# Performance work log

Hardware: AMD Instinct MI355X
Metric: run time of the kernel (lower is better)

Reference implementation:

```python
import jax, jax.numpy as jnp
import numpy as np

N_USER, N_MOVIE, E, H, L = 100000, 20000, 1000000, 64, 2
NEG_SLOPE = 0.2  # PyG GATv2Conv default negative_slope


def _rand_edges(k, n_src, n_dst, e):
    k1, k2 = jax.random.split(k)
    src = jax.random.randint(k1, (e,), 0, n_src, dtype=jnp.int32)
    dst = jax.random.randint(k2, (e,), 0, n_dst, dtype=jnp.int32)
    # ensure no src==dst index collisions so PyG's remove_self_loops is a no-op
    dst = jnp.where(dst == src, (dst + 1) % n_dst, dst)
    return jnp.stack([src, dst])


def setup_inputs() -> dict:
    key = jax.random.key(0)
    ks = jax.random.split(key, 8)
    return {
        "x_user": jax.random.normal(ks[0], (N_USER, H), jnp.float32),
        "x_movie": jax.random.normal(ks[1], (N_MOVIE, H), jnp.float32),
        "edge_u2m": _rand_edges(ks[2], N_USER, N_MOVIE, E),
        "edge_m2u": _rand_edges(ks[3], N_MOVIE, N_USER, E),
        # params stacked as [layer, edge_type, ...]; edge_type 0 = user->movie, 1 = movie->user
        "Wl": jax.random.normal(ks[4], (L, 2, H, H), jnp.float32) / np.sqrt(H).astype(np.float32),
        "bl": jnp.zeros((L, 2, H), jnp.float32),
        "Wr": jax.random.normal(ks[5], (L, 2, H, H), jnp.float32) / np.sqrt(H).astype(np.float32),
        "br": jnp.zeros((L, 2, H), jnp.float32),
        "att": jax.random.normal(ks[6], (L, 2, H), jnp.float32) / np.sqrt(H).astype(np.float32),
        "bias": jnp.zeros((L, 2, H), jnp.float32),
    }


def _segment_softmax(scores, seg, n):
    # numerically-stable softmax over variable-degree dst neighborhoods (PyG softmax)
    m = jax.ops.segment_max(scores, seg, num_segments=n)
    ex = jnp.exp(scores - m[seg])
    s = jax.ops.segment_sum(ex, seg, num_segments=n)
    return ex / (s[seg] + 1e-16)


def _gatv2(x_src, x_dst, edge, Wl, bl, Wr, br, att, bias):
    n_src, n_dst = x_src.shape[0], x_dst.shape[0]
    xl = x_src @ Wl + bl  # [N_src, H]
    xr = x_dst @ Wr + br  # [N_dst, H]
    n_loop = min(n_src, n_dst)  # PyG adds self loops with num_nodes = min(N_src, N_dst)
    loop = jnp.arange(n_loop, dtype=edge.dtype)
    src = jnp.concatenate([edge[0], loop])
    dst = jnp.concatenate([edge[1], loop])
    e = jax.nn.leaky_relu(xl[src] + xr[dst], NEG_SLOPE)  # [E', H] gathered per edge
    score = e @ att  # [E']
    alpha = _segment_softmax(score, dst, n_dst)
    out = jax.ops.segment_sum(xl[src] * alpha[:, None], dst, num_segments=n_dst)
    return out + bias


def reference(x_user, x_movie, edge_u2m, edge_m2u, Wl, bl, Wr, br, att, bias):
    for l in range(L):
        new_movie = _gatv2(x_user, x_movie, edge_u2m,
                           Wl[l, 0], bl[l, 0], Wr[l, 0], br[l, 0], att[l, 0], bias[l, 0])
        new_user = _gatv2(x_movie, x_user, edge_m2u,
                          Wl[l, 1], bl[l, 1], Wr[l, 1], br[l, 1], att[l, 1], bias[l, 1])
        x_movie = jax.nn.selu(new_movie)
        x_user = jax.nn.selu(new_user)
    return x_user, x_movie
```

## Files before the change

kernel.cpp:

```cpp
#include <hip/hip_runtime.h>
#include <hip/hip_fp16.h>
#include <cstdint>

#define H 64
#define EPR 16
#define NB 120

__device__ __forceinline__ float selu_f(float x) {
  const float sc = 1.0507009873554805f;
  const float al = 1.6732632423543772f;
  return x > 0.f ? sc * x : sc * al * (expf(x) - 1.f);
}

__global__ __launch_bounds__(256) void gemm64_dual(
    const float* __restrict__ A,
    const float* __restrict__ W0, const float* __restrict__ b0,
    const float* __restrict__ W1, const float* __restrict__ b1,
    __half* __restrict__ C0, float* __restrict__ C1, int N) {
  __shared__ float Ws0[64 * 64];
  __shared__ float Ws1[64 * 64];
  __shared__ float As[64][65];
  __shared__ float bs0[64], bs1[64];

  const int tid = threadIdx.x;
  for (int i = tid; i < 1024; i += 256) {
    ((float4*)Ws0)[i] = ((const float4*)W0)[i];
    ((float4*)Ws1)[i] = ((const float4*)W1)[i];
  }
  if (tid < 64) { bs0[tid] = b0[tid]; bs1[tid] = b1[tid]; }

  const int row0 = blockIdx.x * 64;
  for (int i = tid; i < 1024; i += 256) {
    int r = i >> 4, c4 = i & 15;
    int row = row0 + r;
    float4 v = make_float4(0.f, 0.f, 0.f, 0.f);
    if (row < N) v = ((const float4*)(A + (size_t)row * H))[c4];
    As[r][c4 * 4 + 0] = v.x;
    As[r][c4 * 4 + 1] = v.y;
    As[r][c4 * 4 + 2] = v.z;
    As[r][c4 * 4 + 3] = v.w;
  }
  __syncthreads();

  const int g = tid & 3;
  const int r = tid >> 2;
  float a0[16], a1[16];
#pragma unroll
  for (int j = 0; j < 16; ++j) { a0[j] = bs0[g * 16 + j]; a1[j] = bs1[g * 16 + j]; }

  for (int k = 0; k < 64; ++k) {
    float ak = As[r][k];
    const float4* w0r = (const float4*)&Ws0[k * 64 + g * 16];
    const float4* w1r = (const float4*)&Ws1[k * 64 + g * 16];
#pragma unroll
    for (int j4 = 0; j4 < 4; ++j4) {
      float4 w0 = w0r[j4], w1 = w1r[j4];
      a0[j4 * 4 + 0] += ak * w0.x; a0[j4 * 4 + 1] += ak * w0.y;
      a0[j4 * 4 + 2] += ak * w0.z; a0[j4 * 4 + 3] += ak * w0.w;
      a1[j4 * 4 + 0] += ak * w1.x; a1[j4 * 4 + 1] += ak * w1.y;
      a1[j4 * 4 + 2] += ak * w1.z; a1[j4 * 4 + 3] += ak * w1.w;
    }
  }

  const int row = row0 + r;
  if (row < N) {
    unsigned pu[8];
#pragma unroll
    for (int j2 = 0; j2 < 8; ++j2) {
      __half2 t = __floats2half2_rn(a0[2 * j2], a0[2 * j2 + 1]);
      pu[j2] = *(unsigned*)&t;
    }
    uint4* c0 = (uint4*)(C0 + (size_t)row * H + g * 16);
    c0[0] = make_uint4(pu[0], pu[1], pu[2], pu[3]);
    c0[1] = make_uint4(pu[4], pu[5], pu[6], pu[7]);

    float4* c1 = (float4*)(C1 + (size_t)row * H + g * 16);
#pragma unroll
    for (int j4 = 0; j4 < 4; ++j4) {
      c1[j4] = make_float4(a1[j4 * 4 + 0], a1[j4 * 4 + 1], a1[j4 * 4 + 2], a1[j4 * 4 + 3]);
    }
  }
}

__global__ __launch_bounds__(256) void bucket_hist(
    const int* __restrict__ ed1, int E1r, int n1e, int sh1, int B1, int* __restrict__ mat1,
    const int* __restrict__ ed2, int E2r, int n2e, int sh2, int B2, int* __restrict__ mat2) {
  __shared__ int hist[256];
  int b = blockIdx.x;
  const int* ed; int Er, ne, sh, Bn, blk; int* mat;
  if (b < NB) { ed = ed1; Er = E1r; ne = n1e; sh = sh1; Bn = B1; mat = mat1; blk = b; }
  else { ed = ed2; Er = E2r; ne = n2e; sh = sh2; Bn = B2; mat = mat2; blk = b - NB; }
  for (int i = threadIdx.x; i < Bn; i += 256) hist[i] = 0;
  __syncthreads();
  int chunk = (ne + NB - 1) / NB;
  int lo = blk * chunk, hi = lo + chunk;
  if (hi > ne) hi = ne;
  for (int e = lo + threadIdx.x; e < hi; e += 256) {
    int d = (e < Er) ? ed[e] : (e - Er);
    atomicAdd(&hist[d >> sh], 1);
  }
  __syncthreads();
  for (int i = threadIdx.x; i < Bn; i += 256) mat[(size_t)i * NB + blk] = hist[i];
}

__global__ __launch_bounds__(256) void scan_partial2(
    const int* __restrict__ cnt1, int n1, int* __restrict__ psum1, int* __restrict__ bsum1,
    const int* __restrict__ cnt2, int n2, int* __restrict__ psum2, int* __restrict__ bsum2,
    int split) {
  __shared__ int sh[256];
  int b = blockIdx.x;
  const int* cnt; int n; int* psum; int* bsum; int lb;
  if (b < split) { cnt = cnt1; n = n1; psum = psum1; bsum = bsum1; lb = b; }
  else { cnt = cnt2; n = n2; psum = psum2; bsum = bsum2; lb = b - split; }
  int i = lb * 256 + threadIdx.x;
  int tid = threadIdx.x;
  sh[tid] = (i < n) ? cnt[i] : 0;
  __syncthreads();
  for (int off = 1; off < 256; off <<= 1) {
    int t = (tid >= off) ? sh[tid - off] : 0;
    __syncthreads();
    if (tid >= off) sh[tid] += t;
    __syncthreads();
  }
  if (i < n) psum[i] = sh[tid];
  if (tid == 255) bsum[lb] = sh[255];
}

__global__ __launch_bounds__(256) void scan_bsums2(
    int* __restrict__ bsum1, int nb1, int* __restrict__ bsum2, int nb2) {
  __shared__ int sh[256];
  const int tid = threadIdx.x;
  for (int which = 0; which < 2; ++which) {
    int* bsum = which ? bsum2 : bsum1;
    int nb = which ? nb2 : nb1;
    int run = 0;
    for (int start = 0; start < nb; start += 256) {
      int i = start + tid;
      int v = (i < nb) ? bsum[i] : 0;
      __syncthreads();
      sh[tid] = v;
      __syncthreads();
      for (int off = 1; off < 256; off <<= 1) {
        int t = (tid >= off) ? sh[tid - off] : 0;
        __syncthreads();
        if (tid >= off) sh[tid] += t;
        __syncthreads();
      }
      if (i < nb) bsum[i] = run + sh[tid] - v;
      run += sh[255];
      __syncthreads();
    }
  }
}

__global__ __launch_bounds__(256) void finalize_excl2(
    const int* __restrict__ cnt1, const int* __restrict__ psum1,
    const int* __restrict__ bsum1, int n1, int* __restrict__ excl1,
    const int* __restrict__ cnt2, const int* __restrict__ psum2,
    const int* __restrict__ bsum2, int n2, int* __restrict__ excl2, int split) {
  int b = blockIdx.x;
  const int *cnt, *psum, *bsum; int n; int* excl; int lb;
  if (b < split) { cnt = cnt1; psum = psum1; bsum = bsum1; n = n1; excl = excl1; lb = b; }
  else { cnt = cnt2; psum = psum2; bsum = bsum2; n = n2; excl = excl2; lb = b - split; }
  int i = lb * 256 + threadIdx.x;
  if (i >= n) return;
  excl[i] = psum[i] + bsum[lb] - cnt[i];
}

__global__ __launch_bounds__(256) void bucket_part(
    const int* __restrict__ es1, const int* __restrict__ ed1, int E1r, int n1e,
    int sh1, int B1, const int* __restrict__ excl1, unsigned* __restrict__ part1,
    const int* __restrict__ es2, const int* __restrict__ ed2, int E2r, int n2e,
    int sh2, int B2, const int* __restrict__ excl2, unsigned* __restrict__ part2) {
  __shared__ int cur[256];
  int b = blockIdx.x;
  const int *es, *ed, *excl; int Er, ne, sh, Bn, blk; unsigned* part;
  if (b < NB) { es = es1; ed = ed1; Er = E1r; ne = n1e; sh = sh1; Bn = B1; excl = excl1; part = part1; blk = b; }
  else { es = es2; ed = ed2; Er = E2r; ne = n2e; sh = sh2; Bn = B2; excl = excl2; part = part2; blk = b - NB; }
  for (int i = threadIdx.x; i < Bn; i += 256) cur[i] = excl[(size_t)i * NB + blk];
  __syncthreads();
  int chunk = (ne + NB - 1) / NB;
  int lo = blk * chunk, hi = lo + chunk;
  if (hi > ne) hi = ne;
  const unsigned lmask = (1u << sh) - 1u;
  for (int e = lo + threadIdx.x; e < hi; e += 256) {
    int s, d;
    if (e < Er) { s = es[e]; d = ed[e]; } else { s = e - Er; d = s; }
    int bkt = d >> sh;
    int pos = atomicAdd(&cur[bkt], 1);
    part[pos] = (((unsigned)d & lmask) << 18) | (unsigned)s;
  }
}

__global__ __launch_bounds__(256) void bucket_sort(
    const unsigned* __restrict__ part1, const int* __restrict__ excl1,
    int n1e, int sh1, int B1, int nd1, int* __restrict__ rp1, int* __restrict__ csr1,
    const unsigned* __restrict__ part2, const int* __restrict__ excl2,
    int n2e, int sh2, int B2, int nd2, int* __restrict__ rp2, int* __restrict__ csr2) {
  __shared__ int cnt_s[512];
  __shared__ int scan_s[512];
  int b = blockIdx.x;
  const unsigned* part; const int* excl; int ne, sh, Bn, nd, bkt; int *rp, *csr;
  if (b < B1) { part = part1; excl = excl1; ne = n1e; sh = sh1; Bn = B1; nd = nd1; rp = rp1; csr = csr1; bkt = b; }
  else { part = part2; excl = excl2; ne = n2e; sh = sh2; Bn = B2; nd = nd2; rp = rp2; csr = csr2; bkt = b - B1; }
  const int tid = threadIdx.x;
  const int dbase = bkt << sh;
  const int R = 1 << sh;
  int rcap = nd - dbase;
  if (rcap > R) rcap = R;
  const int base = excl[(size_t)bkt * NB];
  const int endv = (bkt == Bn - 1) ? ne : excl[(size_t)(bkt + 1) * NB];

  cnt_s[tid] = 0; cnt_s[256 + tid] = 0;
  __syncthreads();
  for (int i = base + tid; i < endv; i += 256)
    atomicAdd(&cnt_s[part[i] >> 18], 1);
  __syncthreads();
  scan_s[tid] = cnt_s[tid];
  scan_s[256 + tid] = cnt_s[256 + tid];
  __syncthreads();
  for (int off = 1; off < 256; off <<= 1) {
    int t = (tid >= off) ? scan_s[tid - off] : 0;
    __syncthreads();
    if (tid >= off) scan_s[tid] += t;
    __syncthreads();
  }
  for (int off = 1; off < 256; off <<= 1) {
    int t = (tid >= off) ? scan_s[256 + tid - off] : 0;
    __syncthreads();
    if (tid >= off) scan_s[256 + tid] += t;
    __syncthreads();
  }
  int lowtot = scan_s[255];
  scan_s[256 + tid] += lowtot;
  __syncthreads();
  if (tid < rcap) rp[dbase + tid + 1] = base + scan_s[tid];
  if (256 + tid < rcap) rp[dbase + 256 + tid + 1] = base + scan_s[256 + tid];
  cnt_s[tid] = base + scan_s[tid] - cnt_s[tid];
  cnt_s[256 + tid] = base + scan_s[256 + tid] - cnt_s[256 + tid];
  if (tid == 0 && bkt == 0) rp[0] = 0;
  __syncthreads();
  for (int i = base + tid; i < endv; i += 256) {
    unsigned p = part[i];
    int dl = p >> 18;
    int pos = atomicAdd(&cnt_s[dl], 1);
    csr[pos] = (int)(p & 0x3FFFFu);
  }
}

__global__ __launch_bounds__(256) void gat_dst(
    const int* __restrict__ row_ptr, const int* __restrict__ csr_src,
    const __half* __restrict__ xl, const float* __restrict__ xr,
    const float* __restrict__ att, const float* __restrict__ bias,
    float* __restrict__ out, int n_dst) {
  __shared__ __align__(16) float tile[4][EPR * 64];

  const int w = threadIdx.x >> 6;
  const int d = blockIdx.x * 4 + w;
  if (d >= n_dst) return;
  const int h = threadIdx.x & 63;
  float* tl = tile[w];

  const float xr_h = xr[(size_t)d * H + h];
  const float att_h = att[h];
  const int beg = row_ptr[d];
  const int end = row_ptr[d + 1];

  const int r = h & 15;
  const int q = h >> 4;

  float m = -3.0e38f, s = 0.f, acc = 0.f;

  for (int base = beg; base < end; base += EPR) {
    int cnt = end - base;
    if (cnt > EPR) cnt = EPR;
    float v[EPR];

#pragma unroll
    for (int qq = 0; qq < EPR / 4; ++qq) {
      if (qq * 4 < cnt) {
#pragma unroll
        for (int i = 0; i < 4; ++i) {
          const int k = qq * 4 + i;
          int j = k < cnt ? k : cnt - 1;
          int src = csr_src[base + j];
          float vv = __half2float(xl[(size_t)src * H + h]);
          v[k] = vv;
          float p = vv + xr_h;
          p = fmaxf(p, 0.f) + 0.2f * fminf(p, 0.f);
          tl[(k << 6) + ((((h >> 2) ^ k) << 2) | (h & 3))] = p * att_h;
        }
      }
    }

    const float4* t4 = (const float4*)tl;
    float t0 = 0.f, t1 = 0.f, t2 = 0.f, t3 = 0.f;
#pragma unroll
    for (int c = 0; c < 4; ++c) {
      float4 q4 = t4[(r << 4) + (((q << 2) + c) ^ r)];
      t0 += q4.x; t1 += q4.y; t2 += q4.z; t3 += q4.w;
    }
    float t = (t0 + t1) + (t2 + t3);
    t += __shfl_xor(t, 16, 64);
    t += __shfl_xor(t, 32, 64);
    t = (r < cnt) ? t : -3.0e38f;

    float M = t;
#pragma unroll
    for (int mk = 1; mk <= 8; mk <<= 1) M = fmaxf(M, __shfl_xor(M, mk, 64));
    float e = __expf(t - M);
    float S = e;
#pragma unroll
    for (int mk = 1; mk <= 8; mk <<= 1) S += __shfl_xor(S, mk, 64);
    if (h < 16) tl[h] = e;

    float nm = fmaxf(m, M);
    float a_old = __expf(m - nm);
    float a_new = __expf(M - nm);
    float P = 0.f;
#pragma unroll
    for (int qq = 0; qq < EPR / 4; ++qq) {
      if (qq * 4 < cnt) {
        float4 w4 = ((const float4*)tl)[qq];
        P += w4.x * v[qq * 4 + 0];
        P += w4.y * v[qq * 4 + 1];
        P += w4.z * v[qq * 4 + 2];
        P += w4.w * v[qq * 4 + 3];
      }
    }
    s = s * a_old + S * a_new;
    acc = acc * a_old + P * a_new;
    m = nm;
  }

  float o = acc / (s + 1e-16f) + bias[h];
  out[(size_t)d * H + h] = selu_f(o);
}

extern "C" void kernel_launch(void* const* d_in, const int* in_sizes, int n_in,
                              void* d_out, int out_size, void* d_ws, size_t ws_size,
                              hipStream_t stream) {
  const float* x_user = (const float*)d_in[0];
  const float* x_movie = (const float*)d_in[1];
  const int* e_u2m = (const int*)d_in[2];
  const int* e_m2u = (const int*)d_in[3];
  const float* Wl = (const float*)d_in[4];
  const float* bl = (const float*)d_in[5];
  const float* Wr = (const float*)d_in[6];
  const float* br = (const float*)d_in[7];
  const float* att = (const float*)d_in[8];
  const float* bias = (const float*)d_in[9];

  const int n_user = in_sizes[0] / H;
  const int n_movie = in_sizes[1] / H;
  const int E1 = in_sizes[2] / 2;
  const int E2 = in_sizes[3] / 2;
  const int n_loop = n_user < n_movie ? n_user : n_movie;
  const int nE1 = E1 + n_loop;
  const int nE2 = E2 + n_loop;

  const int SHM = 7, SHU = 9;
  const int Bm = (n_movie + (1 << SHM) - 1) >> SHM;
  const int Bu = (n_user + (1 << SHU) - 1) >> SHU;
  const int nmatM = Bm * NB, nmatU = Bu * NB;
  const int nbm = (nmatM + 255) / 256, nbu = (nmatU + 255) / 256;

  float* ws = (float*)d_ws;
  size_t o = 0;
  __half* xl_u2m = (__half*)(ws + o); o += (size_t)n_user * H / 2;
  __half* xl_m2u = (__half*)(ws + o); o += (size_t)n_movie * H / 2;
  float* xr_u2m = ws + o; o += (size_t)n_movie * H;
  float* xr_m2u = ws + o; o += (size_t)n_user * H;

  int* matM  = (int*)(ws + o); o += nmatM;
  int* psumM = (int*)(ws + o); o += nmatM;
  int* exclM = (int*)(ws + o); o += nmatM;
  int* matU  = (int*)(ws + o); o += nmatU;
  int* psumU = (int*)(ws + o); o += nmatU;
  int* exclU = (int*)(ws + o); o += nmatU;
  int* bsumM = (int*)(ws + o); o += 1024;
  int* bsumU = (int*)(ws + o); o += 1024;
  unsigned* partM = (unsigned*)(ws + o); o += nE1;
  unsigned* partU = (unsigned*)(ws + o); o += nE2;
  int* csr1 = (int*)(ws + o); o += nE1;
  int* csr2 = (int*)(ws + o); o += nE2;
  int* rp1  = (int*)(ws + o); o += n_movie + 1;
  int* rp2  = (int*)(ws + o); o += n_user + 1;

  float* out_u = (float*)d_out;
  float* out_m = out_u + (size_t)n_user * H;

  const int gu = (n_user + 63) / 64;
  const int gm = (n_movie + 63) / 64;

  bucket_hist<<<2 * NB, 256, 0, stream>>>(
      e_u2m + E1, E1, nE1, SHM, Bm, matM,
      e_m2u + E2, E2, nE2, SHU, Bu, matU);
  scan_partial2<<<nbm + nbu, 256, 0, stream>>>(
      matM, nmatM, psumM, bsumM, matU, nmatU, psumU, bsumU, nbm);
  scan_bsums2<<<1, 256, 0, stream>>>(bsumM, nbm, bsumU, nbu);
  finalize_excl2<<<nbm + nbu, 256, 0, stream>>>(
      matM, psumM, bsumM, nmatM, exclM,
      matU, psumU, bsumU, nmatU, exclU, nbm);
  bucket_part<<<2 * NB, 256, 0, stream>>>(
      e_u2m, e_u2m + E1, E1, nE1, SHM, Bm, exclM, partM,
      e_m2u, e_m2u + E2, E2, nE2, SHU, Bu, exclU, partU);
  bucket_sort<<<Bm + Bu, 256, 0, stream>>>(
      partM, exclM, nE1, SHM, Bm, n_movie, rp1, csr1,
      partU, exclU, nE2, SHU, Bu, n_user, rp2, csr2);

  for (int l = 0; l < 2; ++l) {
    const float* cu = (l == 0) ? x_user : out_u;
    const float* cm = (l == 0) ? x_movie : out_m;
    const int p0 = l * 2 + 0;
    const int p1 = l * 2 + 1;

    gemm64_dual<<<gu, 256, 0, stream>>>(
        cu, Wl + (size_t)p0 * H * H, bl + (size_t)p0 * H,
        Wr + (size_t)p1 * H * H, br + (size_t)p1 * H, xl_u2m, xr_m2u, n_user);
    gemm64_dual<<<gm, 256, 0, stream>>>(
        cm, Wl + (size_t)p1 * H * H, bl + (size_t)p1 * H,
        Wr + (size_t)p0 * H * H, br + (size_t)p0 * H, xl_m2u, xr_u2m, n_movie);

    gat_dst<<<(n_movie + 3) / 4, 256, 0, stream>>>(
        rp1, csr1, xl_u2m, xr_u2m, att + (size_t)p0 * H, bias + (size_t)p0 * H, out_m, n_movie);
    gat_dst<<<(n_user + 3) / 4, 256, 0, stream>>>(
        rp2, csr2, xl_m2u, xr_m2u, att + (size_t)p1 * H, bias + (size_t)p1 * H, out_u, n_user);
  }
}
```

Baseline: 531.5 us.

## Merge per-direction GEMM and GAT launches into single kernels, simplify leaky-relu

Both gemm64_dual calls are fused into one launch and both gat_dst calls into one launch, with each block choosing its edge direction by block index. This cuts launch count and lets the smaller movie-side work fill the GPU alongside the user side, removing tail idle time between launches. Inside the GAT kernel the leaky-relu-times-att is rewritten as a single fma with an abs term, the source index is made wave-uniform via readfirstlane, and the swizzle index math is simplified. The cost is extra pointer selection per block and some divergence in register pressure between the two branches.

```diff
diff --git a/kernel.cpp b/kernel.cpp
--- a/kernel.cpp
+++ b/kernel.cpp
@@ -12,16 +12,30 @@
   return x > 0.f ? sc * x : sc * al * (expf(x) - 1.f);
 }
 
-__global__ __launch_bounds__(256) void gemm64_dual(
-    const float* __restrict__ A,
-    const float* __restrict__ W0, const float* __restrict__ b0,
-    const float* __restrict__ W1, const float* __restrict__ b1,
-    __half* __restrict__ C0, float* __restrict__ C1, int N) {
+__global__ __launch_bounds__(256) void gemm64_dual2(
+    const float* __restrict__ Au, const float* __restrict__ Am,
+    const float* __restrict__ W0u, const float* __restrict__ b0u,
+    const float* __restrict__ W1u, const float* __restrict__ b1u,
+    const float* __restrict__ W0m, const float* __restrict__ b0m,
+    const float* __restrict__ W1m, const float* __restrict__ b1m,
+    __half* __restrict__ C0u, float* __restrict__ C1u,
+    __half* __restrict__ C0m, float* __restrict__ C1m,
+    int Nu, int Nm, int split) {
   __shared__ float Ws0[64 * 64];
   __shared__ float Ws1[64 * 64];
   __shared__ float As[64][65];
   __shared__ float bs0[64], bs1[64];
 
+  const float *A, *W0, *b0, *W1, *b1;
+  __half* C0; float* C1; int N, blk;
+  if (blockIdx.x < split) {
+    A = Au; W0 = W0u; b0 = b0u; W1 = W1u; b1 = b1u;
+    C0 = C0u; C1 = C1u; N = Nu; blk = blockIdx.x;
+  } else {
+    A = Am; W0 = W0m; b0 = b0m; W1 = W1m; b1 = b1m;
+    C0 = C0m; C1 = C1m; N = Nm; blk = blockIdx.x - split;
+  }
+
   const int tid = threadIdx.x;
   for (int i = tid; i < 1024; i += 256) {
     ((float4*)Ws0)[i] = ((const float4*)W0)[i];
@@ -29,7 +43,7 @@
   }
   if (tid < 64) { bs0[tid] = b0[tid]; bs1[tid] = b1[tid]; }
 
-  const int row0 = blockIdx.x * 64;
+  const int row0 = blk * 64;
   for (int i = tid; i < 1024; i += 256) {
     int r = i >> 4, c4 = i & 15;
     int row = row0 + r;
@@ -248,26 +262,43 @@
   }
 }
 
-__global__ __launch_bounds__(256) void gat_dst(
-    const int* __restrict__ row_ptr, const int* __restrict__ csr_src,
-    const __half* __restrict__ xl, const float* __restrict__ xr,
-    const float* __restrict__ att, const float* __restrict__ bias,
-    float* __restrict__ out, int n_dst) {
+__global__ __launch_bounds__(256) void gat_dst2(
+    const int* __restrict__ rp1, const int* __restrict__ csr1,
+    const __half* __restrict__ xl1, const float* __restrict__ xr1,
+    const float* __restrict__ att1, const float* __restrict__ bias1,
+    float* __restrict__ out1, int nd1,
+    const int* __restrict__ rp2, const int* __restrict__ csr2,
+    const __half* __restrict__ xl2, const float* __restrict__ xr2,
+    const float* __restrict__ att2, const float* __restrict__ bias2,
+    float* __restrict__ out2, int nd2, int split) {
   __shared__ __align__(16) float tile[4][EPR * 64];
 
+  const int b = blockIdx.x;
+  const int* rp; const int* csr; const __half* xl; const float *xr, *att, *bias;
+  float* out; int nd, d0;
+  if (b < split) {
+    rp = rp1; csr = csr1; xl = xl1; xr = xr1; att = att1; bias = bias1;
+    out = out1; nd = nd1; d0 = b * 4;
+  } else {
+    rp = rp2; csr = csr2; xl = xl2; xr = xr2; att = att2; bias = bias2;
+    out = out2; nd = nd2; d0 = (b - split) * 4;
+  }
   const int w = threadIdx.x >> 6;
-  const int d = blockIdx.x * 4 + w;
-  if (d >= n_dst) return;
+  const int d = d0 + w;
+  if (d >= nd) return;
   const int h = threadIdx.x & 63;
   float* tl = tile[w];
 
   const float xr_h = xr[(size_t)d * H + h];
-  const float att_h = att[h];
-  const int beg = row_ptr[d];
-  const int end = row_ptr[d + 1];
+  const float a = att[h];
+  const float a06 = 0.6f * a, a04 = 0.4f * a;
+  const float bias_h = bias[h];
+  const int beg = rp[d];
+  const int end = rp[d + 1];
 
   const int r = h & 15;
   const int q = h >> 4;
+  const int pr = (q << 2) ^ r;
 
   float m = -3.0e38f, s = 0.f, acc = 0.f;
 
@@ -283,12 +314,13 @@
         for (int i = 0; i < 4; ++i) {
           const int k = qq * 4 + i;
           int j = k < cnt ? k : cnt - 1;
-          int src = csr_src[base + j];
-          float vv = __half2float(xl[(size_t)src * H + h]);
+          int src = __builtin_amdgcn_readfirstlane(csr[base + j]);
+          const __half* row = xl + ((size_t)src << 6);
+          float vv = __half2float(row[h]);
           v[k] = vv;
           float p = vv + xr_h;
-          p = fmaxf(p, 0.f) + 0.2f * fminf(p, 0.f);
-          tl[(k << 6) + ((((h >> 2) ^ k) << 2) | (h & 3))] = p * att_h;
+          float c = fmaf(p, a06, fabsf(p) * a04);
+          tl[(k << 6) | (h ^ (k << 2))] = c;
         }
       }
     }
@@ -297,7 +329,7 @@
     float t0 = 0.f, t1 = 0.f, t2 = 0.f, t3 = 0.f;
 #pragma unroll
     for (int c = 0; c < 4; ++c) {
-      float4 q4 = t4[(r << 4) + (((q << 2) + c) ^ r)];
+      float4 q4 = t4[(r << 4) | (pr ^ c)];
       t0 += q4.x; t1 += q4.y; t2 += q4.z; t3 += q4.w;
     }
     float t = (t0 + t1) + (t2 + t3);
@@ -333,7 +365,7 @@
     m = nm;
   }
 
-  float o = acc / (s + 1e-16f) + bias[h];
+  float o = acc / (s + 1e-16f) + bias_h;
   out[(size_t)d * H + h] = selu_f(o);
 }
 
@@ -392,6 +424,8 @@
 
   const int gu = (n_user + 63) / 64;
   const int gm = (n_movie + 63) / 64;
+  const int split1 = (n_movie + 3) / 4;
+  const int split2 = (n_user + 3) / 4;
 
   bucket_hist<<<2 * NB, 256, 0, stream>>>(
       e_u2m + E1, E1, nE1, SHM, Bm, matM,
@@ -415,16 +449,19 @@
     const int p0 = l * 2 + 0;
     const int p1 = l * 2 + 1;
 
-    gemm64_dual<<<gu, 256, 0, stream>>>(
-        cu, Wl + (size_t)p0 * H * H, bl + (size_t)p0 * H,
-        Wr + (size_t)p1 * H * H, br + (size_t)p1 * H, xl_u2m, xr_m2u, n_user);
-    gemm64_dual<<<gm, 256, 0, stream>>>(
-        cm, Wl + (size_t)p1 * H * H, bl + (size_t)p1 * H,
-        Wr + (size_t)p0 * H * H, br + (size_t)p0 * H, xl_m2u, xr_u2m, n_movie);
-
-    gat_dst<<<(n_movie + 3) / 4, 256, 0, stream>>>(
-        rp1, csr1, xl_u2m, xr_u2m, att + (size_t)p0 * H, bias + (size_t)p0 * H, out_m, n_movie);
-    gat_dst<<<(n_user + 3) / 4, 256, 0, stream>>>(
-        rp2, csr2, xl_m2u, xr_m2u, att + (size_t)p1 * H, bias + (size_t)p1 * H, out_u, n_user);
-  }
-}
+    gemm64_dual2<<<gu + gm, 256, 0, stream>>>(
+        cu, cm,
+        Wl + (size_t)p0 * H * H, bl + (size_t)p0 * H,
+        Wr + (size_t)p1 * H * H, br + (size_t)p1 * H,
+        Wl + (size_t)p1 * H * H, bl + (size_t)p1 * H,
+        Wr + (size_t)p0 * H * H, br + (size_t)p0 * H,
+        xl_u2m, xr_m2u, xl_m2u, xr_u2m,
+        n_user, n_movie, gu);
+
+    gat_dst2<<<split1 + split2, 256, 0, stream>>>(
+        rp1, csr1, xl_u2m, xr_u2m, att + (size_t)p0 * H, bias + (size_t)p0 * H,
+        out_m, n_movie,
+        rp2, csr2, xl_m2u, xr_m2u, att + (size_t)p1 * H, bias + (size_t)p1 * H,
+        out_u, n_user, split1);
+  }
+}
```

Measured after the change: 612.8 us. +15.3%, slower.
